# Optimization experiments

Hardware: AMD Instinct MI355X
Metric: run time of the kernel (lower is better)

The kernel has to match this reference:

```python
import jax, jax.numpy as jnp
import numpy as np

N = 100000
E = 1600000
IN_C, HID_C, OUT_C = 128, 64, 40


def setup_inputs() -> dict:
    key = jax.random.key(0)
    ks = jax.random.split(key, 9)
    x = jax.random.normal(ks[0], (N, IN_C), dtype=jnp.float32)
    src = jax.random.randint(ks[1], (E,), 0, N, dtype=jnp.int64)
    dst = jax.random.randint(ks[2], (E,), 0, N, dtype=jnp.int64)
    edge_index = jnp.stack([src, dst], axis=0)
    def glorot(k, fan_in, fan_out):
        s = jnp.sqrt(6.0 / (fan_in + fan_out)).astype(jnp.float32)
        return jax.random.uniform(k, (fan_in, fan_out), jnp.float32, -s, s)
    return {
        "x": x,
        "edge_index": edge_index,
        "W1": glorot(ks[3], IN_C, HID_C), "b1": jnp.zeros((HID_C,), jnp.float32),
        "W2": glorot(ks[4], HID_C, HID_C), "b2": jnp.zeros((HID_C,), jnp.float32),
        "W3": glorot(ks[5], HID_C, OUT_C), "b3": jnp.zeros((OUT_C,), jnp.float32),
    }


def _gcn_norm(edge_index, n_nodes):
    # add self-loops, then symmetric normalization D^-1/2 (A+I) D^-1/2
    loops = jnp.arange(n_nodes, dtype=edge_index.dtype)
    src = jnp.concatenate([edge_index[0], loops])
    dst = jnp.concatenate([edge_index[1], loops])
    deg = jax.ops.segment_sum(jnp.ones_like(dst, dtype=jnp.float32), dst,
                              num_segments=n_nodes)
    dinv = jnp.where(deg > 0, jax.lax.rsqrt(deg), 0.0)
    norm = dinv[src] * dinv[dst]  # [E + N]
    return src, dst, norm


def _gcn_conv(h, W, b, src, dst, norm, n_nodes):
    h = h @ W                                   # [N, out]
    msg = norm[:, None] * h[src]                # gather + scale, [E+N, out]
    out = jax.ops.segment_sum(msg, dst, num_segments=n_nodes)  # scatter-add
    return out + b


def reference(x, edge_index, W1, b1, W2, b2, W3, b3):
    n_nodes = x.shape[0]
    src, dst, norm = _gcn_norm(edge_index, n_nodes)
    h = jax.nn.relu(_gcn_conv(x, W1, b1, src, dst, norm, n_nodes))
    # dropout(p=0.5) is identity in eval mode
    h = jax.nn.relu(_gcn_conv(h, W2, b2, src, dst, norm, n_nodes))
    out = _gcn_conv(h, W3, b3, src, dst, norm, n_nodes)
    return out
```

## Files before the change

### kernel.cpp

```cpp
#include <hip/hip_runtime.h>

#define N_NODES 100000
#define N_EDGES 1600000
#define NBUCK 196
#define BCAP 9600
#define CH 4096
#define NCHUNK ((N_EDGES + CH - 1) / CH)

typedef __attribute__((ext_vector_type(2))) _Float16 half2v;
typedef __attribute__((ext_vector_type(4))) _Float16 half4v;
typedef __attribute__((ext_vector_type(8))) _Float16 half8v;
typedef __attribute__((ext_vector_type(4))) float f32x4;

__device__ __forceinline__ float4 loadX4(const float* X, size_t idx) {
    return *(const float4*)(X + idx);
}
__device__ __forceinline__ float4 loadX4(const _Float16* X, size_t idx) {
    half4v h = *(const half4v*)(X + idx);
    return make_float4((float)h.x, (float)h.y, (float)h.z, (float)h.w);
}


__global__ __launch_bounds__(256) void zero_small(int* p, int n) {
    int i = blockIdx.x * blockDim.x + threadIdx.x;
    if (i < n) p[i] = 0;
}

__global__ __launch_bounds__(256) void multisplit(const int* __restrict__ src,
                                                  const int* __restrict__ dst,
                                                  int* cursor,
                                                  int* __restrict__ bucketed, int e) {
    __shared__ int cnt[NBUCK];
    __shared__ int basel[NBUCK];
    const int t = threadIdx.x;
    const int base_e = blockIdx.x * CH;

    int myS[16], myD[16];
    for (int i = t; i < NBUCK; i += 256) cnt[i] = 0;
    __syncthreads();

#pragma unroll
    for (int k = 0; k < 16; ++k) {
        int i = base_e + k * 256 + t;
        if (i < e) {
            myS[k] = src[i];
            myD[k] = dst[i];
            atomicAdd(&cnt[myD[k] >> 9], 1);
        } else {
            myD[k] = -1;
        }
    }
    __syncthreads();
    for (int i = t; i < NBUCK; i += 256) basel[i] = atomicAdd(&cursor[i], cnt[i]);
    __syncthreads();
    for (int i = t; i < NBUCK; i += 256) cnt[i] = 0;
    __syncthreads();

#pragma unroll
    for (int k = 0; k < 16; ++k) {
        if (myD[k] >= 0) {
            int b = myD[k] >> 9;
            int pos = basel[b] + atomicAdd(&cnt[b], 1);
            if (pos < BCAP)
                bucketed[(size_t)b * BCAP + pos] = ((myD[k] & 511) << 17) | myS[k];
        }
    }
}

__global__ __launch_bounds__(256) void bucket_scan(const int* __restrict__ cursor,
                                                   int* __restrict__ gbase) {
    __shared__ int sm[256];
    const int t = threadIdx.x;
    int v = (t < NBUCK) ? cursor[t] : 0;
    sm[t] = v;
    __syncthreads();
    for (int off = 1; off < 256; off <<= 1) {
        int u = (t >= off) ? sm[t - off] : 0;
        __syncthreads();
        sm[t] += u;
        __syncthreads();
    }
    if (t < NBUCK) gbase[t] = sm[t] - v;
    if (t == NBUCK - 1) gbase[NBUCK] = sm[t];
}

__global__ __launch_bounds__(512) void build_csr(const int* __restrict__ bucketed,
                                                 const int* __restrict__ gbase,
                                                 int* __restrict__ row_ptr,
                                                 float* __restrict__ dinv,
                                                 int* __restrict__ csr_src, int n) {
    __shared__ int vals[BCAP];
    __shared__ int cnt[512];
    __shared__ int lcur[512];
    const int b = blockIdx.x;
    const int t = threadIdx.x;
    const int nb0 = b * 512;
    const int nn = min(512, n - nb0);
    const int gb = gbase[b];
    const int m = gbase[b + 1] - gb;

    cnt[t] = 0;
    __syncthreads();
    for (int i = t; i < m; i += 512) {
        int v = bucketed[(size_t)b * BCAP + i];
        vals[i] = v;
        atomicAdd(&cnt[v >> 17], 1);
    }
    __syncthreads();

    int deg = cnt[t];
    for (int off = 1; off < 512; off <<= 1) {
        int u = (t >= off) ? cnt[t - off] : 0;
        __syncthreads();
        cnt[t] += u;
        __syncthreads();
    }
    int offv = cnt[t] - deg;
    __syncthreads();
    cnt[t] = offv;
    lcur[t] = 0;
    if (t < nn) {
        row_ptr[nb0 + t] = gb + offv;
        dinv[nb0 + t] = rsqrtf((float)(deg + 1));
    }
    if (b == NBUCK - 1 && t == 0) row_ptr[n] = gb + m;
    __syncthreads();

    for (int i = t; i < m; i += 512) {
        int v = vals[i];
        int node = v >> 17;
        int pos = atomicAdd(&lcur[node], 1);
        csr_src[gb + cnt[node] + pos] = v & 0x1FFFF;
    }
}


template <int K>
__global__ __launch_bounds__(256) void transpose_w(const float* __restrict__ W,
                                                   _Float16* __restrict__ Wt) {
    int i = blockIdx.x * 256 + threadIdx.x;
    if (i < K * 64) {
        int k = i >> 6, nn = i & 63;
        Wt[(size_t)nn * K + k] = (_Float16)W[i];
    }
}


__device__ __forceinline__ void stageX_rows(const float* X, _Float16* Xl, int t,
                                            int row0, int n, int K, int SP) {
    for (int i = t; i < 64 * K / 4; i += 256) {
        int r = i / (K / 4), c = (i % (K / 4)) * 4;
        int grow = min(row0 + r, n - 1);
        float4 v = *(const float4*)(X + (size_t)grow * K + c);
        half4v h = {(_Float16)v.x, (_Float16)v.y, (_Float16)v.z, (_Float16)v.w};
        *(half4v*)(Xl + r * SP + c) = h;
    }
}
__device__ __forceinline__ void stageX_rows(const _Float16* X, _Float16* Xl, int t,
                                            int row0, int n, int K, int SP) {
    for (int i = t; i < 64 * K / 8; i += 256) {
        int r = i / (K / 8), c = (i % (K / 8)) * 8;
        int grow = min(row0 + r, n - 1);
        *(half8v*)(Xl + r * SP + c) = *(const half8v*)(X + (size_t)grow * K + c);
    }
}

template <int K, typename XT>
__global__ __launch_bounds__(256) void gemm_mfma64(const XT* __restrict__ X,
                                                   const _Float16* __restrict__ Wt,
                                                   const float* __restrict__ dinv,
                                                   _Float16* __restrict__ Y, int n) {
    constexpr int SP = K + 8;
    __shared__ _Float16 Xl[64 * SP];
    __shared__ _Float16 Wl[64 * SP];
    const int t = threadIdx.x;
    const int wave = t >> 6, lane = t & 63;
    const int row0 = blockIdx.x * 64;
    const int m = lane & 15, quad = lane >> 4;

    if (blockIdx.x == 0 && t < 32) ((int*)(Y + (size_t)n * 64))[t] = 0;

    for (int i = t; i < 64 * K / 8; i += 256) {
        int r = i / (K / 8), c = (i % (K / 8)) * 8;
        *(half8v*)(Wl + r * SP + c) = *(const half8v*)(Wt + (size_t)r * K + c);
    }
    stageX_rows(X, Xl, t, row0, n, K, SP);
    __syncthreads();

    f32x4 acc[4] = {{0,0,0,0},{0,0,0,0},{0,0,0,0},{0,0,0,0}};
#pragma unroll
    for (int k0 = 0; k0 < K; k0 += 32) {
        half8v a = *(const half8v*)(Xl + (wave * 16 + m) * SP + k0 + quad * 8);
#pragma unroll
        for (int ct = 0; ct < 4; ++ct) {
            half8v b = *(const half8v*)(Wl + (ct * 16 + m) * SP + k0 + quad * 8);
            acc[ct] = __builtin_amdgcn_mfma_f32_16x16x32_f16(a, b, acc[ct], 0, 0, 0);
        }
    }

    float dv[4];
#pragma unroll
    for (int r = 0; r < 4; ++r) {
        int row = row0 + wave * 16 + quad * 4 + r;
        dv[r] = dinv[min(row, n - 1)];
    }
#pragma unroll
    for (int ct = 0; ct < 4; ++ct) {
#pragma unroll
        for (int r = 0; r < 4; ++r) {
            int row = row0 + wave * 16 + quad * 4 + r;
            if (row < n)
                Y[(size_t)row * 64 + ct * 16 + m] = (_Float16)(dv[r] * acc[ct][r]);
        }
    }
}


template <int K, int COUT, typename XT>
__global__ __launch_bounds__(256) void gemm_rt(const XT* __restrict__ X,
                                               const float* __restrict__ W,
                                               const float* __restrict__ dinv,
                                               _Float16* __restrict__ Y, int n) {
    constexpr int KC = 64;
    constexpr int S = KC + 4;
    constexpr int NCH = K / KC;
    __shared__ float Xl[64 * S];
    __shared__ float Wl[KC * COUT];

    const int t = threadIdx.x;
    const int row0 = blockIdx.x * 64;
    const int cg = (t & 15) * 4;
    const int rg = (t >> 4) * 4;

    if (blockIdx.x == 0 && t < COUT / 2) ((int*)(Y + (size_t)n * COUT))[t] = 0;

    float acc[4][4] = {};

#pragma unroll
    for (int ch = 0; ch < NCH; ++ch) {
        const int k0 = ch * KC;
        for (int i = t; i < 64 * KC / 4; i += 256) {
            int r = i >> 4;
            int k = (i & 15) * 4;
            int grow = min(row0 + r, n - 1);
            *(float4*)(Xl + r * S + k) = loadX4(X, (size_t)grow * K + k0 + k);
        }
        for (int i = t; i < KC * COUT / 4; i += 256) {
            *(float4*)(Wl + i * 4) = *(const float4*)(W + (size_t)k0 * COUT + (size_t)i * 4);
        }
        __syncthreads();

        if (cg < COUT) {
#pragma unroll 4
            for (int k = 0; k < KC; ++k) {
                float4 w = *(const float4*)(Wl + k * COUT + cg);
                float x0 = Xl[(rg + 0) * S + k];
                float x1 = Xl[(rg + 1) * S + k];
                float x2 = Xl[(rg + 2) * S + k];
                float x3 = Xl[(rg + 3) * S + k];
                acc[0][0] += x0 * w.x; acc[0][1] += x0 * w.y; acc[0][2] += x0 * w.z; acc[0][3] += x0 * w.w;
                acc[1][0] += x1 * w.x; acc[1][1] += x1 * w.y; acc[1][2] += x1 * w.z; acc[1][3] += x1 * w.w;
                acc[2][0] += x2 * w.x; acc[2][1] += x2 * w.y; acc[2][2] += x2 * w.z; acc[2][3] += x2 * w.w;
                acc[3][0] += x3 * w.x; acc[3][1] += x3 * w.y; acc[3][2] += x3 * w.z; acc[3][3] += x3 * w.w;
            }
        }
        __syncthreads();
    }

    if (cg < COUT) {
#pragma unroll
        for (int r = 0; r < 4; ++r) {
            int row = row0 + rg + r;
            if (row < n) {
                float d = dinv[row];
                half4v o = { (_Float16)(d * acc[r][0]), (_Float16)(d * acc[r][1]),
                             (_Float16)(d * acc[r][2]), (_Float16)(d * acc[r][3]) };
                *(half4v*)(Y + (size_t)row * COUT + cg) = o;
            }
        }
    }
}


template <bool RELU>
__global__ __launch_bounds__(256) void aggregate64c(const _Float16* __restrict__ tS,
                                                    const int* __restrict__ row_ptr,
                                                    const int* __restrict__ csr_src,
                                                    const float* __restrict__ dinv,
                                                    const float* __restrict__ bias,
                                                    _Float16* __restrict__ out, int n) {
    const int t = threadIdx.x;
    const int lane = t & 63;
    const int c8 = lane & 7;
    const int node = blockIdx.x * 32 + (t >> 3);
    const half8v* tS8 = (const half8v*)tS;
    const int bpb = (lane & 56) << 2;

    const int beg = row_ptr[node];
    const int cnt = row_ptr[node + 1] - beg;
    const int cl = (cnt > 0) ? cnt - 1 : 0;

    int mc = cnt;
    mc = max(mc, __shfl_xor(mc, 8));
    mc = max(mc, __shfl_xor(mc, 16));
    mc = max(mc, __shfl_xor(mc, 32));

    half8v accA, accB;
#pragma unroll
    for (int i = 0; i < 8; ++i) { accA[i] = (_Float16)0; accB[i] = (_Float16)0; }

    for (int j0 = 0; j0 < mc; j0 += 8) {
        int sj = csr_src[beg + min(j0 + c8, cl)];
#pragma unroll
        for (int jj = 0; jj < 8; ++jj) {
            int e = __builtin_amdgcn_ds_bpermute(bpb + jj * 4, sj);
            e = (j0 + jj < cnt) ? e : n;
            half8v v = tS8[(size_t)e * 8 + c8];
            if (jj & 1) accB += v; else accA += v;
        }
    }

    float acc[8];
#pragma unroll
    for (int i = 0; i < 8; ++i) acc[i] = (float)accA[i] + (float)accB[i];

    half8v selfh = tS8[(size_t)node * 8 + c8];
    float4 b0 = ((const float4*)bias)[c8 * 2];
    float4 b1 = ((const float4*)bias)[c8 * 2 + 1];
    const float bb[8] = {b0.x, b0.y, b0.z, b0.w, b1.x, b1.y, b1.z, b1.w};
    float d = dinv[node];
    half8v o;
#pragma unroll
    for (int i = 0; i < 8; ++i) {
        float v = bb[i] + d * (acc[i] + (float)selfh[i]);
        if (RELU) v = fmaxf(v, 0.0f);
        o[i] = (_Float16)v;
    }
    ((half8v*)out)[(size_t)node * 8 + c8] = o;
}


__global__ __launch_bounds__(256) void aggregate40w(const _Float16* __restrict__ tS,
                                                    const int* __restrict__ row_ptr,
                                                    const int* __restrict__ csr_src,
                                                    const float* __restrict__ dinv,
                                                    const float* __restrict__ bias,
                                                    float* __restrict__ out, int n) {
    const int t = threadIdx.x;
    const int lane = t & 63;
    const int wave = t >> 6;
    const int g = lane / 10;
    const int c10 = lane - g * 10;
    const int node = blockIdx.x * 24 + wave * 6 + g;
    const bool act = (g < 6) && (node < n);
    const half4v* tS4 = (const half4v*)tS;
    const int bpb = g * 40;

    const int nclamp = act ? node : 0;
    const int beg = row_ptr[nclamp];
    const int cnt = act ? (row_ptr[nclamp + 1] - beg) : 0;
    const int cl = (cnt > 0) ? cnt - 1 : 0;

    int mc = cnt;
    mc = max(mc, __shfl_xor(mc, 1));
    mc = max(mc, __shfl_xor(mc, 2));
    mc = max(mc, __shfl_xor(mc, 4));
    mc = max(mc, __shfl_xor(mc, 8));
    mc = max(mc, __shfl_xor(mc, 16));
    mc = max(mc, __shfl_xor(mc, 32));

    half4v accA, accB;
#pragma unroll
    for (int i = 0; i < 4; ++i) { accA[i] = (_Float16)0; accB[i] = (_Float16)0; }

    for (int j0 = 0; j0 < mc; j0 += 10) {
        int sj = csr_src[beg + min(j0 + c10, cl)];
#pragma unroll
        for (int jj = 0; jj < 10; ++jj) {
            int e = __builtin_amdgcn_ds_bpermute(bpb + jj * 4, sj);
            e = (j0 + jj < cnt) ? e : n;
            half4v v = tS4[(size_t)e * 10 + c10];
            if (jj & 1) accB += v; else accA += v;
        }
    }

    if (act) {
        float acc[4];
#pragma unroll
        for (int i = 0; i < 4; ++i) acc[i] = (float)accA[i] + (float)accB[i];

        half4v selfh = tS4[(size_t)node * 10 + c10];
        float4 b = ((const float4*)bias)[c10];
        const float bb[4] = {b.x, b.y, b.z, b.w};
        float d = dinv[node];
        float4 o;
        o.x = bb[0] + d * (acc[0] + (float)selfh[0]);
        o.y = bb[1] + d * (acc[1] + (float)selfh[1]);
        o.z = bb[2] + d * (acc[2] + (float)selfh[2]);
        o.w = bb[3] + d * (acc[3] + (float)selfh[3]);
        *(float4*)(out + (size_t)node * 40 + c10 * 4) = o;
    }
}


extern "C" void kernel_launch(void* const* d_in, const int* in_sizes, int n_in,
                              void* d_out, int out_size, void* d_ws, size_t ws_size,
                              hipStream_t stream) {
    const float* x  = (const float*)d_in[0];
    const int*   ei = (const int*)d_in[1];
    const int*   src = ei;
    const int*   dst = ei + N_EDGES;
    const float* W1 = (const float*)d_in[2];
    const float* b1 = (const float*)d_in[3];
    const float* W2 = (const float*)d_in[4];
    const float* b2 = (const float*)d_in[5];
    const float* W3 = (const float*)d_in[6];
    const float* b3 = (const float*)d_in[7];
    float* out = (float*)d_out;

    const int N = N_NODES, E = N_EDGES;

    char* p = (char*)d_ws;
    int*   cursor   = (int*)p;              p += 256 * 4;
    int*   gbase    = (int*)p;              p += 256 * 4;
    float* dinv     = (float*)p;            p += (size_t)N * 4;
    int*   row_ptr  = (int*)p;              p += (size_t)(N + 4) * 4;
    int*   bucketed = (int*)p;              p += (size_t)NBUCK * BCAP * 4;
    int*   csr_src  = (int*)p;              p += (size_t)E * 4;
    p = (char*)(((size_t)p + 15) & ~(size_t)15);
    _Float16* Wt1   = (_Float16*)p;         p += (size_t)64 * 128 * 2;
    _Float16* Wt2   = (_Float16*)p;         p += (size_t)64 * 64 * 2;
    _Float16* bufA  = (_Float16*)p;         p += (size_t)(N + 64) * 64 * 2;
    p = (char*)(((size_t)p + 15) & ~(size_t)15);
    _Float16* bufB  = (_Float16*)p;         p += (size_t)N * 64 * 2;

    zero_small<<<1, 256, 0, stream>>>(cursor, NBUCK);
    transpose_w<128><<<32, 256, 0, stream>>>(W1, Wt1);
    transpose_w<64><<<16, 256, 0, stream>>>(W2, Wt2);
    multisplit<<<NCHUNK, 256, 0, stream>>>(src, dst, cursor, bucketed, E);
    bucket_scan<<<1, 256, 0, stream>>>(cursor, gbase);
    build_csr<<<NBUCK, 512, 0, stream>>>(bucketed, gbase, row_ptr, dinv, csr_src, N);

    const int agg64Grid = N / 32;
    const int agg40Grid = (N + 23) / 24;
    const int gemmGrid = (N + 63) / 64;

    gemm_mfma64<128, float><<<gemmGrid, 256, 0, stream>>>(x, Wt1, dinv, bufA, N);
    aggregate64c<true><<<agg64Grid, 256, 0, stream>>>(bufA, row_ptr, csr_src, dinv, b1, bufB, N);

    gemm_mfma64<64, _Float16><<<gemmGrid, 256, 0, stream>>>(bufB, Wt2, dinv, bufA, N);
    aggregate64c<true><<<agg64Grid, 256, 0, stream>>>(bufA, row_ptr, csr_src, dinv, b2, bufB, N);

    gemm_rt<64, 40, _Float16><<<gemmGrid, 256, 0, stream>>>(bufB, W3, dinv, bufA, N);
    aggregate40w<<<agg40Grid, 256, 0, stream>>>(bufA, row_ptr, csr_src, dinv, b3, out, N);
}
```

Baseline: 311.3 us.

## Slice CSR neighbors by source range and use persistent-grid aggregation

The CSR build now sub-sorts each node's neighbor list into 7 source-index slices and stores 8 offsets per node. The aggregation kernels walk the slices in order under a persistent grid of 1024 blocks, so concurrently running blocks gather from a similar range of feature rows and can reuse them in L2. This adds per-slice loop overhead, divergence from uneven slice counts (about 2 edges per slice), and a larger offset array.

```diff
diff --git a/kernel.cpp b/kernel.cpp
--- a/kernel.cpp
+++ b/kernel.cpp
@@ -6,6 +6,9 @@
 #define BCAP 9600
 #define CH 4096
 #define NCHUNK ((N_EDGES + CH - 1) / CH)
+#define SLICE_SH 14
+#define NSLICE 7
+#define GRID_AGG 1024
 
 typedef __attribute__((ext_vector_type(2))) _Float16 half2v;
 typedef __attribute__((ext_vector_type(4))) _Float16 half4v;
@@ -86,12 +89,12 @@
 
 __global__ __launch_bounds__(512) void build_csr(const int* __restrict__ bucketed,
                                                  const int* __restrict__ gbase,
-                                                 int* __restrict__ row_ptr,
+                                                 int* __restrict__ off2,
                                                  float* __restrict__ dinv,
                                                  int* __restrict__ csr_src, int n) {
     __shared__ int vals[BCAP];
+    __shared__ int cnt2[512 * 8];
     __shared__ int cnt[512];
-    __shared__ int lcur[512];
     const int b = blockIdx.x;
     const int t = threadIdx.x;
     const int nb0 = b * 512;
@@ -99,38 +102,50 @@
     const int gb = gbase[b];
     const int m = gbase[b + 1] - gb;
 
-    cnt[t] = 0;
+    for (int i = t; i < 512 * 8; i += 512) cnt2[i] = 0;
     __syncthreads();
     for (int i = t; i < m; i += 512) {
         int v = bucketed[(size_t)b * BCAP + i];
         vals[i] = v;
-        atomicAdd(&cnt[v >> 17], 1);
-    }
-    __syncthreads();
-
-    int deg = cnt[t];
+        int s = (v & 0x1FFFF) >> SLICE_SH;
+        atomicAdd(&cnt2[(v >> 17) * 8 + s], 1);
+    }
+    __syncthreads();
+
+    int c[8];
+    int deg = 0;
+#pragma unroll
+    for (int s = 0; s < 8; ++s) {
+        int d = cnt2[t * 8 + s];
+        c[s] = deg;
+        deg += d;
+    }
+    cnt[t] = deg;
+    __syncthreads();
     for (int off = 1; off < 512; off <<= 1) {
         int u = (t >= off) ? cnt[t - off] : 0;
         __syncthreads();
         cnt[t] += u;
         __syncthreads();
     }
-    int offv = cnt[t] - deg;
-    __syncthreads();
-    cnt[t] = offv;
-    lcur[t] = 0;
+    const int nodebase = cnt[t] - deg;
+    const int abase = gb + nodebase;
+#pragma unroll
+    for (int s = 0; s < 8; ++s) cnt2[t * 8 + s] = abase + c[s];
     if (t < nn) {
-        row_ptr[nb0 + t] = gb + offv;
+#pragma unroll
+        for (int s = 0; s < 7; ++s) off2[(size_t)(nb0 + t) * 8 + s] = abase + c[s];
+        off2[(size_t)(nb0 + t) * 8 + 7] = abase + deg;
         dinv[nb0 + t] = rsqrtf((float)(deg + 1));
     }
-    if (b == NBUCK - 1 && t == 0) row_ptr[n] = gb + m;
     __syncthreads();
 
     for (int i = t; i < m; i += 512) {
         int v = vals[i];
-        int node = v >> 17;
-        int pos = atomicAdd(&lcur[node], 1);
-        csr_src[gb + cnt[node] + pos] = v & 0x1FFFF;
+        int src = v & 0x1FFFF;
+        int s = src >> SLICE_SH;
+        int pos = atomicAdd(&cnt2[(v >> 17) * 8 + s], 1);
+        csr_src[pos] = src;
     }
 }
 
@@ -283,8 +298,8 @@
 
 
 template <bool RELU>
-__global__ __launch_bounds__(256) void aggregate64c(const _Float16* __restrict__ tS,
-                                                    const int* __restrict__ row_ptr,
+__global__ __launch_bounds__(256) void aggregate64s(const _Float16* __restrict__ tS,
+                                                    const int* __restrict__ off2,
                                                     const int* __restrict__ csr_src,
                                                     const float* __restrict__ dinv,
                                                     const float* __restrict__ bias,
@@ -292,56 +307,62 @@
     const int t = threadIdx.x;
     const int lane = t & 63;
     const int c8 = lane & 7;
-    const int node = blockIdx.x * 32 + (t >> 3);
     const half8v* tS8 = (const half8v*)tS;
     const int bpb = (lane & 56) << 2;
 
-    const int beg = row_ptr[node];
-    const int cnt = row_ptr[node + 1] - beg;
-    const int cl = (cnt > 0) ? cnt - 1 : 0;
-
-    int mc = cnt;
-    mc = max(mc, __shfl_xor(mc, 8));
-    mc = max(mc, __shfl_xor(mc, 16));
-    mc = max(mc, __shfl_xor(mc, 32));
-
-    half8v accA, accB;
-#pragma unroll
-    for (int i = 0; i < 8; ++i) { accA[i] = (_Float16)0; accB[i] = (_Float16)0; }
-
-    for (int j0 = 0; j0 < mc; j0 += 8) {
-        int sj = csr_src[beg + min(j0 + c8, cl)];
-#pragma unroll
-        for (int jj = 0; jj < 8; ++jj) {
-            int e = __builtin_amdgcn_ds_bpermute(bpb + jj * 4, sj);
-            e = (j0 + jj < cnt) ? e : n;
-            half8v v = tS8[(size_t)e * 8 + c8];
-            if (jj & 1) accB += v; else accA += v;
-        }
-    }
-
-    float acc[8];
-#pragma unroll
-    for (int i = 0; i < 8; ++i) acc[i] = (float)accA[i] + (float)accB[i];
-
-    half8v selfh = tS8[(size_t)node * 8 + c8];
     float4 b0 = ((const float4*)bias)[c8 * 2];
     float4 b1 = ((const float4*)bias)[c8 * 2 + 1];
     const float bb[8] = {b0.x, b0.y, b0.z, b0.w, b1.x, b1.y, b1.z, b1.w};
-    float d = dinv[node];
-    half8v o;
-#pragma unroll
-    for (int i = 0; i < 8; ++i) {
-        float v = bb[i] + d * (acc[i] + (float)selfh[i]);
-        if (RELU) v = fmaxf(v, 0.0f);
-        o[i] = (_Float16)v;
-    }
-    ((half8v*)out)[(size_t)node * 8 + c8] = o;
-}
-
-
-__global__ __launch_bounds__(256) void aggregate40w(const _Float16* __restrict__ tS,
-                                                    const int* __restrict__ row_ptr,
+
+    for (int chunk = blockIdx.x; chunk < N_NODES / 32; chunk += GRID_AGG) {
+        const int node = chunk * 32 + (t >> 3);
+        int myoff = off2[(size_t)node * 8 + c8];
+
+        half8v acc0, acc1;
+#pragma unroll
+        for (int i = 0; i < 8; ++i) { acc0[i] = (_Float16)0; acc1[i] = (_Float16)0; }
+
+        for (int s = 0; s < NSLICE; ++s) {
+            int beg = __builtin_amdgcn_ds_bpermute(bpb + s * 4, myoff);
+            int end = __builtin_amdgcn_ds_bpermute(bpb + s * 4 + 4, myoff);
+            int cnt = end - beg;
+            int mc = cnt;
+            mc = max(mc, __shfl_xor(mc, 8));
+            mc = max(mc, __shfl_xor(mc, 16));
+            mc = max(mc, __shfl_xor(mc, 32));
+            int cl = (cnt > 0) ? cnt - 1 : 0;
+            for (int j0 = 0; j0 < mc; j0 += 8) {
+                int sj = csr_src[beg + min(j0 + c8, cl)];
+#pragma unroll
+                for (int jj = 0; jj < 8; ++jj) {
+                    int e = __builtin_amdgcn_ds_bpermute(bpb + jj * 4, sj);
+                    e = (j0 + jj < cnt) ? e : n;
+                    half8v v = tS8[(size_t)e * 8 + c8];
+                    if (jj & 1) acc1 += v; else acc0 += v;
+                }
+            }
+        }
+
+        float acc[8];
+#pragma unroll
+        for (int i = 0; i < 8; ++i) acc[i] = (float)acc0[i] + (float)acc1[i];
+
+        half8v selfh = tS8[(size_t)node * 8 + c8];
+        float d = dinv[node];
+        half8v o;
+#pragma unroll
+        for (int i = 0; i < 8; ++i) {
+            float v = bb[i] + d * (acc[i] + (float)selfh[i]);
+            if (RELU) v = fmaxf(v, 0.0f);
+            o[i] = (_Float16)v;
+        }
+        ((half8v*)out)[(size_t)node * 8 + c8] = o;
+    }
+}
+
+
+__global__ __launch_bounds__(256) void aggregate40s(const _Float16* __restrict__ tS,
+                                                    const int* __restrict__ off2,
                                                     const int* __restrict__ csr_src,
                                                     const float* __restrict__ dinv,
                                                     const float* __restrict__ bias,
@@ -351,54 +372,60 @@
     const int wave = t >> 6;
     const int g = lane / 10;
     const int c10 = lane - g * 10;
-    const int node = blockIdx.x * 24 + wave * 6 + g;
-    const bool act = (g < 6) && (node < n);
     const half4v* tS4 = (const half4v*)tS;
     const int bpb = g * 40;
 
-    const int nclamp = act ? node : 0;
-    const int beg = row_ptr[nclamp];
-    const int cnt = act ? (row_ptr[nclamp + 1] - beg) : 0;
-    const int cl = (cnt > 0) ? cnt - 1 : 0;
-
-    int mc = cnt;
-    mc = max(mc, __shfl_xor(mc, 1));
-    mc = max(mc, __shfl_xor(mc, 2));
-    mc = max(mc, __shfl_xor(mc, 4));
-    mc = max(mc, __shfl_xor(mc, 8));
-    mc = max(mc, __shfl_xor(mc, 16));
-    mc = max(mc, __shfl_xor(mc, 32));
-
-    half4v accA, accB;
-#pragma unroll
-    for (int i = 0; i < 4; ++i) { accA[i] = (_Float16)0; accB[i] = (_Float16)0; }
-
-    for (int j0 = 0; j0 < mc; j0 += 10) {
-        int sj = csr_src[beg + min(j0 + c10, cl)];
-#pragma unroll
-        for (int jj = 0; jj < 10; ++jj) {
-            int e = __builtin_amdgcn_ds_bpermute(bpb + jj * 4, sj);
-            e = (j0 + jj < cnt) ? e : n;
-            half4v v = tS4[(size_t)e * 10 + c10];
-            if (jj & 1) accB += v; else accA += v;
-        }
-    }
-
-    if (act) {
-        float acc[4];
-#pragma unroll
-        for (int i = 0; i < 4; ++i) acc[i] = (float)accA[i] + (float)accB[i];
-
-        half4v selfh = tS4[(size_t)node * 10 + c10];
-        float4 b = ((const float4*)bias)[c10];
-        const float bb[4] = {b.x, b.y, b.z, b.w};
-        float d = dinv[node];
-        float4 o;
-        o.x = bb[0] + d * (acc[0] + (float)selfh[0]);
-        o.y = bb[1] + d * (acc[1] + (float)selfh[1]);
-        o.z = bb[2] + d * (acc[2] + (float)selfh[2]);
-        o.w = bb[3] + d * (acc[3] + (float)selfh[3]);
-        *(float4*)(out + (size_t)node * 40 + c10 * 4) = o;
+    const int nchunk40 = (N_NODES + 23) / 24;
+
+    for (int chunk = blockIdx.x; chunk < nchunk40; chunk += GRID_AGG) {
+        const int node = chunk * 24 + wave * 6 + g;
+        const bool act = (g < 6) && (node < n);
+        const int nclamp = act ? node : 0;
+        int myoff = (c10 < 8) ? off2[(size_t)nclamp * 8 + c10] : 0;
+
+        half4v a0, a1;
+#pragma unroll
+        for (int i = 0; i < 4; ++i) { a0[i] = (_Float16)0; a1[i] = (_Float16)0; }
+
+        for (int s = 0; s < NSLICE; ++s) {
+            int beg = __builtin_amdgcn_ds_bpermute(bpb + s * 4, myoff);
+            int end = __builtin_amdgcn_ds_bpermute(bpb + s * 4 + 4, myoff);
+            int cnt = act ? (end - beg) : 0;
+            int mc = cnt;
+            mc = max(mc, __shfl_xor(mc, 1));
+            mc = max(mc, __shfl_xor(mc, 2));
+            mc = max(mc, __shfl_xor(mc, 4));
+            mc = max(mc, __shfl_xor(mc, 8));
+            mc = max(mc, __shfl_xor(mc, 16));
+            mc = max(mc, __shfl_xor(mc, 32));
+            int cl = (cnt > 0) ? cnt - 1 : 0;
+            for (int j0 = 0; j0 < mc; j0 += 10) {
+                int sj = csr_src[beg + min(j0 + c10, cl)];
+#pragma unroll
+                for (int jj = 0; jj < 10; ++jj) {
+                    int e = __builtin_amdgcn_ds_bpermute(bpb + jj * 4, sj);
+                    e = (j0 + jj < cnt) ? e : n;
+                    half4v v = tS4[(size_t)e * 10 + c10];
+                    if (jj & 1) a1 += v; else a0 += v;
+                }
+            }
+        }
+
+        if (act) {
+            float acc[4];
+#pragma unroll
+            for (int i = 0; i < 4; ++i) acc[i] = (float)a0[i] + (float)a1[i];
+
+            half4v selfh = tS4[(size_t)node * 10 + c10];
+            float4 b = ((const float4*)bias)[c10];
+            float d = dinv[node];
+            float4 o;
+            o.x = b.x + d * (acc[0] + (float)selfh[0]);
+            o.y = b.y + d * (acc[1] + (float)selfh[1]);
+            o.z = b.z + d * (acc[2] + (float)selfh[2]);
+            o.w = b.w + d * (acc[3] + (float)selfh[3]);
+            *(float4*)(out + (size_t)node * 40 + c10 * 4) = o;
+        }
     }
 }
 
@@ -424,9 +451,9 @@
     int*   cursor   = (int*)p;              p += 256 * 4;
     int*   gbase    = (int*)p;              p += 256 * 4;
     float* dinv     = (float*)p;            p += (size_t)N * 4;
-    int*   row_ptr  = (int*)p;              p += (size_t)(N + 4) * 4;
+    int*   off2     = (int*)p;              p += (size_t)N * 8 * 4;
     int*   bucketed = (int*)p;              p += (size_t)NBUCK * BCAP * 4;
-    int*   csr_src  = (int*)p;              p += (size_t)E * 4;
+    int*   csr_src  = (int*)p;              p += (size_t)(E + 64) * 4;
     p = (char*)(((size_t)p + 15) & ~(size_t)15);
     _Float16* Wt1   = (_Float16*)p;         p += (size_t)64 * 128 * 2;
     _Float16* Wt2   = (_Float16*)p;         p += (size_t)64 * 64 * 2;
@@ -439,18 +466,16 @@
     transpose_w<64><<<16, 256, 0, stream>>>(W2, Wt2);
     multisplit<<<NCHUNK, 256, 0, stream>>>(src, dst, cursor, bucketed, E);
     bucket_scan<<<1, 256, 0, stream>>>(cursor, gbase);
-    build_csr<<<NBUCK, 512, 0, stream>>>(bucketed, gbase, row_ptr, dinv, csr_src, N);
-
-    const int agg64Grid = N / 32;
-    const int agg40Grid = (N + 23) / 24;
+    build_csr<<<NBUCK, 512, 0, stream>>>(bucketed, gbase, off2, dinv, csr_src, N);
+
     const int gemmGrid = (N + 63) / 64;
 
     gemm_mfma64<128, float><<<gemmGrid, 256, 0, stream>>>(x, Wt1, dinv, bufA, N);
-    aggregate64c<true><<<agg64Grid, 256, 0, stream>>>(bufA, row_ptr, csr_src, dinv, b1, bufB, N);
+    aggregate64s<true><<<GRID_AGG, 256, 0, stream>>>(bufA, off2, csr_src, dinv, b1, bufB, N);
 
     gemm_mfma64<64, _Float16><<<gemmGrid, 256, 0, stream>>>(bufB, Wt2, dinv, bufA, N);
-    aggregate64c<true><<<agg64Grid, 256, 0, stream>>>(bufA, row_ptr, csr_src, dinv, b2, bufB, N);
+    aggregate64s<true><<<GRID_AGG, 256, 0, stream>>>(bufA, off2, csr_src, dinv, b2, bufB, N);
 
     gemm_rt<64, 40, _Float16><<<gemmGrid, 256, 0, stream>>>(bufB, W3, dinv, bufA, N);
-    aggregate40w<<<agg40Grid, 256, 0, stream>>>(bufA, row_ptr, csr_src, dinv, b3, out, N);
-}
+    aggregate40s<<<GRID_AGG, 256, 0, stream>>>(bufA, off2, csr_src, dinv, b3, out, N);
+}
```

Measured after the change: 396.1 us. +27.2%, slower.
